# Optimization experiments

Measured on AMD Instinct MI355X. Metric: run time of the kernel, lower is better.

The kernel has to match this reference:

```python
import jax, jax.numpy as jnp
import numpy as np

GRID_H = 64
GRID_W = 64


def make_grid(h, w):
    # torch.meshgrid([arange(h), arange(w)], indexing='xy') -> shape (w, h);
    # grid[i, j] = (j + 0.5, i + 0.5). With h == w == 64 this is square.
    gx, gy = jnp.meshgrid(jnp.arange(h, dtype=jnp.float32),
                          jnp.arange(w, dtype=jnp.float32), indexing='xy')
    return jnp.stack([gx, gy], axis=-1) + 0.5  # (w, h, 2)


def setup_inputs() -> dict:
    key = jax.random.key(0)
    k1, k2 = jax.random.split(key)
    x = jax.random.normal(k1, (4, 128, 64, 64), dtype=jnp.float32)
    y = jax.random.normal(k2, (4, 128, 64, 64), dtype=jnp.float32)
    return {"x": x, "y": y}


def reference(x, y):
    b, c, hx, wx = x.shape
    _, _, hy, wy = y.shape
    scale = c ** (-0.5)
    grids = make_grid(GRID_H, GRID_W)[:hy, :wy].reshape(-1, 2)  # (hy*wy, 2)

    x_ = x.reshape(b, c, hx * wx)
    y_ = y.reshape(b, c, hy * wy)
    # (b, q, k) attention over all key pixels
    attn = jax.nn.softmax(jnp.einsum('bcq,bck->bqk', x_, y_) * scale, axis=-1)
    uv = jnp.einsum('bqk,kt->bqt', attn, grids)  # (b, hx*wx, 2)
    uv = uv.reshape(b, hx, wx, 2)
    # normalize to [-1, 1]
    norm = jnp.asarray([wy, hy], dtype=uv.dtype)
    uv = uv / norm * 2.0 - 1.0
    return uv
```

## Files before the change

### kernel.cpp

```cpp
#include <hip/hip_runtime.h>
#include <math.h>

typedef __attribute__((ext_vector_type(8))) _Float16 f16x8;
typedef __attribute__((ext_vector_type(4))) float f32x4;

#define NPIX 4096
#define C_DIM 128
#define SCALE2 0.12752064638518208f

#if __has_builtin(__builtin_amdgcn_exp2f)
#define EXP2(x) __builtin_amdgcn_exp2f(x)
#else
#define EXP2(x) exp2f(x)
#endif

#define WS_NEED ((size_t)4 << 20)

__global__ __launch_bounds__(256) void conv_y(const float* __restrict__ y,
                                              char* __restrict__ ws)
{
    __shared__ float T[32][132];
    const int wg  = blockIdx.x;
    const int xcd = wg & 7;
    const int b   = xcd >> 1;
    const int sl  = ((xcd & 1) << 6) | (wg >> 3);
    const int k0  = sl * 32;
    const int t   = threadIdx.x;

    {
        const int c = t >> 1, half = t & 1;
        const float* srow = y + ((size_t)b * C_DIM + c) * NPIX + k0 + half * 16;
        float4 rv[4];
        #pragma unroll
        for (int u = 0; u < 4; ++u) rv[u] = *(const float4*)(srow + u * 4);
        #pragma unroll
        for (int u = 0; u < 4; ++u) {
            T[half * 16 + u * 4 + 0][c] = rv[u].x;
            T[half * 16 + u * 4 + 1][c] = rv[u].y;
            T[half * 16 + u * 4 + 2][c] = rv[u].z;
            T[half * 16 + u * 4 + 3][c] = rv[u].w;
        }
    }
    __syncthreads();

    char* panel = ws + (size_t)b * (NPIX * 256);
    const int k = t >> 3, g2 = t & 7;
    f16x8 v0, v1;
    #pragma unroll
    for (int m = 0; m < 8; ++m) {
        v0[m] = (_Float16)T[k][g2 * 16 + m];
        v1[m] = (_Float16)T[k][g2 * 16 + 8 + m];
    }
    const int key = k0 + k, s = key & 7;
    char* drow = panel + (size_t)key * 256;
    *(f16x8*)(drow + (((2 * g2)     ^ s) << 4)) = v0;
    *(f16x8*)(drow + (((2 * g2 + 1) ^ s) << 4)) = v1;
}

__global__ __launch_bounds__(512) void uv_main(const char* __restrict__ ws,
                                               const float* __restrict__ x,
                                               float* __restrict__ out)
{
    __shared__ __align__(16) char Ys[3][32768];

    const int t = threadIdx.x, w = t >> 6, l = t & 63;
    const int n16 = l & 15, quad = l >> 4;
    const int wg  = blockIdx.x;
    const int xcd = wg & 7;
    const int b   = xcd >> 1;
    const int qt  = ((xcd & 1) << 5) | (wg >> 3);
    const int q0  = qt * 64;

    f16x8 bx[4][4];
    {
        const float* xq = x + (size_t)b * C_DIM * NPIX + q0 + n16;
        #pragma unroll
        for (int cc = 0; cc < 4; ++cc)
            #pragma unroll
            for (int qg = 0; qg < 4; ++qg) {
                f16x8 hh;
                #pragma unroll
                for (int j = 0; j < 8; ++j)
                    hh[j] = (_Float16)(xq[(size_t)(cc * 32 + quad * 8 + j) * NPIX + qg * 16] * SCALE2);
                bx[cc][qg] = hh;
            }
    }

    const char* panel = ws + (size_t)b * (NPIX * 256);

    const int arow = w * 16 + n16;
    int aoff[4];
    #pragma unroll
    for (int cc = 0; cc < 4; ++cc)
        aoff[cc] = arow * 256 + (((cc * 4 + quad) ^ (n16 & 7)) << 4);

    int soff[4];
    #pragma unroll
    for (int i = 0; i < 4; ++i) soff[i] = (w * 16 + i * 4) * 256 + l * 16;

    #pragma unroll
    for (int pb = 0; pb < 2; ++pb) {
        const char* gt = panel + (size_t)pb * 32768;
        #pragma unroll
        for (int i = 0; i < 4; ++i)
            __builtin_amdgcn_global_load_lds(
                (const __attribute__((address_space(1))) void*)(gt + soff[i]),
                (__attribute__((address_space(3))) void*)(&Ys[pb][soff[i]]), 16, 0, 0);
    }

    float gxv[4];
    #pragma unroll
    for (int r = 0; r < 4; ++r) gxv[r] = (float)((w & 3) * 16 + quad * 4 + r) + 0.5f;
    const float gyw = (float)(w >> 2) + 0.5f;
    float den[4] = {0.f, 0.f, 0.f, 0.f}, nu[4] = {0.f, 0.f, 0.f, 0.f}, nv[4] = {0.f, 0.f, 0.f, 0.f};

    int bufc = 0;
    for (int kt = 0; kt < 32; ++kt) {
        char* cur = Ys[bufc];

        if (kt < 30) {
            int bufn = bufc + 2; if (bufn >= 3) bufn -= 3;
            const char* gt = panel + (size_t)(kt + 2) * 32768;
            char* nb = Ys[bufn];
            #pragma unroll
            for (int i = 0; i < 4; ++i)
                __builtin_amdgcn_global_load_lds(
                    (const __attribute__((address_space(1))) void*)(gt + soff[i]),
                    (__attribute__((address_space(3))) void*)(&nb[soff[i]]), 16, 0, 0);
            __builtin_amdgcn_s_waitcnt(0x0F78);
        } else {
            __builtin_amdgcn_s_waitcnt(0x0F70);
        }

        f32x4 acc[4];
        #pragma unroll
        for (int qg = 0; qg < 4; ++qg) acc[qg] = (f32x4){0.f, 0.f, 0.f, 0.f};

        #pragma unroll
        for (int cc = 0; cc < 4; ++cc) {
            const f16x8 A = *(const f16x8*)(cur + aoff[cc]);
            #pragma unroll
            for (int qg = 0; qg < 4; ++qg)
                acc[qg] = __builtin_amdgcn_mfma_f32_16x16x32_f16(A, bx[cc][qg], acc[qg], 0, 0, 0);
        }

        const float gy = 2.0f * (float)kt + gyw;
        #pragma unroll
        for (int qg = 0; qg < 4; ++qg) {
            float ps = 0.f, pc = 0.f;
            #pragma unroll
            for (int r = 0; r < 4; ++r) {
                const float p = EXP2(acc[qg][r]);
                ps += p;
                pc += p * gxv[r];
            }
            den[qg] += ps;
            nu[qg]  += pc;
            nv[qg]  += gy * ps;
        }
        ++bufc; if (bufc >= 3) bufc -= 3;
    }

    #pragma unroll
    for (int qg = 0; qg < 4; ++qg) {
        #pragma unroll
        for (int mk = 16; mk <= 32; mk <<= 1) {
            den[qg] += __shfl_xor(den[qg], mk);
            nu[qg]  += __shfl_xor(nu[qg],  mk);
            nv[qg]  += __shfl_xor(nv[qg],  mk);
        }
    }
    __syncthreads();
    float* red = (float*)&Ys[0][0];
    if (quad == 0) {
        #pragma unroll
        for (int qg = 0; qg < 4; ++qg) {
            const int base = (w * 64 + qg * 16 + n16) * 3;
            red[base + 0] = den[qg];
            red[base + 1] = nu[qg];
            red[base + 2] = nv[qg];
        }
    }
    __syncthreads();
    if (t < 64) {
        float d = 0.f, u = 0.f, v = 0.f;
        #pragma unroll
        for (int ww = 0; ww < 8; ++ww) {
            d += red[(ww * 64 + t) * 3 + 0];
            u += red[(ww * 64 + t) * 3 + 1];
            v += red[(ww * 64 + t) * 3 + 2];
        }
        const float inv = 1.0f / d;
        *(float2*)(out + ((size_t)b * NPIX + q0 + t) * 2) =
            make_float2(u * inv * 0.03125f - 1.0f, v * inv * 0.03125f - 1.0f);
    }
}

__global__ __launch_bounds__(256, 2) void uv_attn_kernel(
    const float* __restrict__ x, const float* __restrict__ y, float* __restrict__ out)
{
    __shared__ float Xs[C_DIM][32];
    __shared__ float Ysf[64][128];
    const float SCALE = 0.08838834764831845f;
    const int tid = threadIdx.x;
    const int wgid = blockIdx.x;
    const int xcd = wgid & 7;
    const int b = xcd & 3;
    const int q0 = (((xcd >> 2) << 6) | (wgid >> 3)) * 32;
    const float* xb = x + (size_t)b * C_DIM * NPIX + q0;
    {
        const int cr = tid >> 3;
        const int cc = (tid & 7) << 2;
        #pragma unroll
        for (int i = 0; i < 4; ++i) {
            float4 v = *(const float4*)(xb + (size_t)(cr + (i << 5)) * NPIX + cc);
            v.x *= SCALE; v.y *= SCALE; v.z *= SCALE; v.w *= SCALE;
            *(float4*)(&Xs[cr + (i << 5)][cc]) = v;
        }
    }
    const int rg = tid >> 4;
    const int lane16 = tid & 15;
    const int r0 = rg << 1;
    const int col0 = lane16 << 3;
    float gxv[8];
    #pragma unroll
    for (int j2 = 0; j2 < 8; ++j2) gxv[j2] = (float)((col0 & 63) + j2) + 0.5f;
    const float gyb = (float)(lane16 >> 3) + 0.5f;
    float m_run[2] = {-INFINITY, -INFINITY};
    float den[2] = {0.f, 0.f}, nu[2] = {0.f, 0.f}, nv[2] = {0.f, 0.f};
    const int yr = tid >> 5;
    const int yc = (tid & 31) << 2;
    const float* ybase = y + (size_t)b * C_DIM * NPIX;
    for (int kt = 0; kt < 32; ++kt) {
        float S[2][8];
        #pragma unroll
        for (int r = 0; r < 2; ++r)
            #pragma unroll
            for (int j2 = 0; j2 < 8; ++j2) S[r][j2] = 0.f;
        #pragma unroll
        for (int cb = 0; cb < 2; ++cb) {
            __syncthreads();
            const float* yt = ybase + (size_t)(cb << 6) * NPIX + kt * 128;
            #pragma unroll
            for (int i = 0; i < 8; ++i)
                *(float4*)(&Ysf[yr + (i << 3)][yc]) =
                    *(const float4*)(yt + (size_t)(yr + (i << 3)) * NPIX + yc);
            __syncthreads();
            const int cbase = cb << 6;
            #pragma unroll 16
            for (int c = 0; c < 64; ++c) {
                const float2 xa = *(const float2*)(&Xs[cbase + c][r0]);
                const float4 ya = *(const float4*)(&Ysf[c][col0]);
                const float4 yb4 = *(const float4*)(&Ysf[c][col0 + 4]);
                S[0][0] += xa.x * ya.x;  S[0][1] += xa.x * ya.y;
                S[0][2] += xa.x * ya.z;  S[0][3] += xa.x * ya.w;
                S[0][4] += xa.x * yb4.x; S[0][5] += xa.x * yb4.y;
                S[0][6] += xa.x * yb4.z; S[0][7] += xa.x * yb4.w;
                S[1][0] += xa.y * ya.x;  S[1][1] += xa.y * ya.y;
                S[1][2] += xa.y * ya.z;  S[1][3] += xa.y * ya.w;
                S[1][4] += xa.y * yb4.x; S[1][5] += xa.y * yb4.y;
                S[1][6] += xa.y * yb4.z; S[1][7] += xa.y * yb4.w;
            }
        }
        const float gy = gyb + 2.0f * (float)kt;
        #pragma unroll
        for (int r = 0; r < 2; ++r) {
            float tmax = S[r][0];
            #pragma unroll
            for (int j2 = 1; j2 < 8; ++j2) tmax = fmaxf(tmax, S[r][j2]);
            #pragma unroll
            for (int mk = 8; mk >= 1; mk >>= 1) tmax = fmaxf(tmax, __shfl_xor(tmax, mk, 16));
            const float mnew = fmaxf(m_run[r], tmax);
            const float alpha = __expf(m_run[r] - mnew);
            m_run[r] = mnew;
            float psum = 0.f, pu = 0.f;
            #pragma unroll
            for (int j2 = 0; j2 < 8; ++j2) {
                const float p = __expf(S[r][j2] - mnew);
                psum += p; pu += p * gxv[j2];
            }
            den[r] = den[r] * alpha + psum;
            nu[r] = nu[r] * alpha + pu;
            nv[r] = nv[r] * alpha + gy * psum;
        }
    }
    #pragma unroll
    for (int r = 0; r < 2; ++r)
        #pragma unroll
        for (int mk = 8; mk >= 1; mk >>= 1) {
            den[r] += __shfl_xor(den[r], mk, 16);
            nu[r] += __shfl_xor(nu[r], mk, 16);
            nv[r] += __shfl_xor(nv[r], mk, 16);
        }
    if (lane16 == 0) {
        #pragma unroll
        for (int r = 0; r < 2; ++r) {
            const float inv = 1.0f / den[r];
            const int q = q0 + r0 + r;
            *(float2*)(out + ((size_t)b * NPIX + q) * 2) =
                make_float2(nu[r] * inv * 0.03125f - 1.0f, nv[r] * inv * 0.03125f - 1.0f);
        }
    }
}

extern "C" void kernel_launch(void* const* d_in, const int* in_sizes, int n_in,
                              void* d_out, int out_size, void* d_ws, size_t ws_size,
                              hipStream_t stream) {
    const float* x = (const float*)d_in[0];
    const float* y = (const float*)d_in[1];
    float* out = (float*)d_out;
    if (ws_size >= WS_NEED) {
        hipLaunchKernelGGL(conv_y, dim3(512), dim3(256), 0, stream, y, (char*)d_ws);
        hipLaunchKernelGGL(uv_main, dim3(256), dim3(512), 0, stream,
                           (const char*)d_ws, x, out);
    } else {
        hipLaunchKernelGGL(uv_attn_kernel, dim3(512), dim3(256), 0, stream, x, y, out);
    }
}
```

Baseline: 90.77 us.

## Pre-convert x to fp16 panels and replicate y panels per XCD

After: 97.32 us. 7.2% more time.

```diff
diff --git a/kernel.cpp b/kernel.cpp
--- a/kernel.cpp
+++ b/kernel.cpp
@@ -14,22 +14,30 @@
 #define EXP2(x) exp2f(x)
 #endif
 
-#define WS_NEED ((size_t)4 << 20)
-
-__global__ __launch_bounds__(256) void conv_y(const float* __restrict__ y,
-                                              char* __restrict__ ws)
+#define WS_XP  ((size_t)8 << 20)
+#define WS_NEED ((size_t)12 << 20)
+
+__global__ __launch_bounds__(256) void conv_all(const float* __restrict__ x,
+                                                const float* __restrict__ y,
+                                                char* __restrict__ ws)
 {
     __shared__ float T[32][132];
-    const int wg  = blockIdx.x;
-    const int xcd = wg & 7;
+    const int id  = blockIdx.x;
+    const int isX = (id >= 1024);
+    const int id2 = isX ? (id - 1024) : id;
+    const int xcd = id2 & 7;
     const int b   = xcd >> 1;
-    const int sl  = ((xcd & 1) << 6) | (wg >> 3);
+    const int sl  = isX ? (((xcd & 1) << 6) | (id2 >> 3)) : (id2 >> 3);
     const int k0  = sl * 32;
-    const int t   = threadIdx.x;
+    const float* src = isX ? x : y;
+    char* dst = isX ? (ws + WS_XP + (size_t)b * (1 << 20))
+                    : (ws + (size_t)xcd * (1 << 20));
+    const float sc = isX ? SCALE2 : 1.0f;
+    const int t = threadIdx.x;
 
     {
         const int c = t >> 1, half = t & 1;
-        const float* srow = y + ((size_t)b * C_DIM + c) * NPIX + k0 + half * 16;
+        const float* srow = src + ((size_t)b * C_DIM + c) * NPIX + k0 + half * 16;
         float4 rv[4];
         #pragma unroll
         for (int u = 0; u < 4; ++u) rv[u] = *(const float4*)(srow + u * 4);
@@ -43,22 +51,21 @@
     }
     __syncthreads();
 
-    char* panel = ws + (size_t)b * (NPIX * 256);
     const int k = t >> 3, g2 = t & 7;
     f16x8 v0, v1;
     #pragma unroll
     for (int m = 0; m < 8; ++m) {
-        v0[m] = (_Float16)T[k][g2 * 16 + m];
-        v1[m] = (_Float16)T[k][g2 * 16 + 8 + m];
-    }
-    const int key = k0 + k, s = key & 7;
-    char* drow = panel + (size_t)key * 256;
+        v0[m] = (_Float16)(T[k][g2 * 16 + m] * sc);
+        v1[m] = (_Float16)(T[k][g2 * 16 + 8 + m] * sc);
+    }
+    const int key = k0 + k;
+    const int s = isX ? 0 : (key & 7);
+    char* drow = dst + (size_t)key * 256;
     *(f16x8*)(drow + (((2 * g2)     ^ s) << 4)) = v0;
     *(f16x8*)(drow + (((2 * g2 + 1) ^ s) << 4)) = v1;
 }
 
 __global__ __launch_bounds__(512) void uv_main(const char* __restrict__ ws,
-                                               const float* __restrict__ x,
                                                float* __restrict__ out)
 {
     __shared__ __align__(16) char Ys[3][32768];
@@ -71,22 +78,16 @@
     const int qt  = ((xcd & 1) << 5) | (wg >> 3);
     const int q0  = qt * 64;
 
+    const char* xp = ws + WS_XP + (size_t)b * (1 << 20) + (size_t)q0 * 256;
     f16x8 bx[4][4];
-    {
-        const float* xq = x + (size_t)b * C_DIM * NPIX + q0 + n16;
-        #pragma unroll
-        for (int cc = 0; cc < 4; ++cc)
-            #pragma unroll
-            for (int qg = 0; qg < 4; ++qg) {
-                f16x8 hh;
-                #pragma unroll
-                for (int j = 0; j < 8; ++j)
-                    hh[j] = (_Float16)(xq[(size_t)(cc * 32 + quad * 8 + j) * NPIX + qg * 16] * SCALE2);
-                bx[cc][qg] = hh;
-            }
-    }
-
-    const char* panel = ws + (size_t)b * (NPIX * 256);
+    #pragma unroll
+    for (int cc = 0; cc < 4; ++cc)
+        #pragma unroll
+        for (int qg = 0; qg < 4; ++qg)
+            bx[cc][qg] = *(const f16x8*)(xp + (size_t)(qg * 16 + n16) * 256
+                                            + (cc * 4 + quad) * 16);
+
+    const char* panel = ws + (size_t)xcd * (1 << 20);
 
     const int arow = w * 16 + n16;
     int aoff[4];
@@ -310,9 +311,9 @@
     const float* y = (const float*)d_in[1];
     float* out = (float*)d_out;
     if (ws_size >= WS_NEED) {
-        hipLaunchKernelGGL(conv_y, dim3(512), dim3(256), 0, stream, y, (char*)d_ws);
+        hipLaunchKernelGGL(conv_all, dim3(1536), dim3(256), 0, stream, x, y, (char*)d_ws);
         hipLaunchKernelGGL(uv_main, dim3(256), dim3(512), 0, stream,
-                           (const char*)d_ws, x, out);
+                           (const char*)d_ws, out);
     } else {
         hipLaunchKernelGGL(uv_attn_kernel, dim3(512), dim3(256), 0, stream, x, y, out);
     }
```

## Load key operand directly from global into registers instead of LDS staging

Applied to the files above, without the earlier changes.

Measured after the change: 98.65 us. +8.7%, slower.

```diff
diff --git a/kernel.cpp b/kernel.cpp
--- a/kernel.cpp
+++ b/kernel.cpp
@@ -51,17 +51,16 @@
         v0[m] = (_Float16)T[k][g2 * 16 + m];
         v1[m] = (_Float16)T[k][g2 * 16 + 8 + m];
     }
-    const int key = k0 + k, s = key & 7;
-    char* drow = panel + (size_t)key * 256;
-    *(f16x8*)(drow + (((2 * g2)     ^ s) << 4)) = v0;
-    *(f16x8*)(drow + (((2 * g2 + 1) ^ s) << 4)) = v1;
+    char* drow = panel + (size_t)(k0 + k) * 256;
+    *(f16x8*)(drow + (2 * g2)     * 16) = v0;
+    *(f16x8*)(drow + (2 * g2 + 1) * 16) = v1;
 }
 
 __global__ __launch_bounds__(512) void uv_main(const char* __restrict__ ws,
                                                const float* __restrict__ x,
                                                float* __restrict__ out)
 {
-    __shared__ __align__(16) char Ys[3][32768];
+    __shared__ float red[8 * 64 * 3];
 
     const int t = threadIdx.x, w = t >> 6, l = t & 63;
     const int n16 = l & 15, quad = l >> 4;
@@ -86,27 +85,13 @@
             }
     }
 
-    const char* panel = ws + (size_t)b * (NPIX * 256);
-
-    const int arow = w * 16 + n16;
-    int aoff[4];
+    const char* ap = ws + (size_t)b * (NPIX * 256)
+                   + (size_t)((w * 16 + n16) * 256 + quad * 16);
+
+    f16x8 Ab[2][4];
     #pragma unroll
     for (int cc = 0; cc < 4; ++cc)
-        aoff[cc] = arow * 256 + (((cc * 4 + quad) ^ (n16 & 7)) << 4);
-
-    int soff[4];
-    #pragma unroll
-    for (int i = 0; i < 4; ++i) soff[i] = (w * 16 + i * 4) * 256 + l * 16;
-
-    #pragma unroll
-    for (int pb = 0; pb < 2; ++pb) {
-        const char* gt = panel + (size_t)pb * 32768;
-        #pragma unroll
-        for (int i = 0; i < 4; ++i)
-            __builtin_amdgcn_global_load_lds(
-                (const __attribute__((address_space(1))) void*)(gt + soff[i]),
-                (__attribute__((address_space(3))) void*)(&Ys[pb][soff[i]]), 16, 0, 0);
-    }
+        Ab[0][cc] = *(const f16x8*)(ap + cc * 64);
 
     float gxv[4];
     #pragma unroll
@@ -114,22 +99,15 @@
     const float gyw = (float)(w >> 2) + 0.5f;
     float den[4] = {0.f, 0.f, 0.f, 0.f}, nu[4] = {0.f, 0.f, 0.f, 0.f}, nv[4] = {0.f, 0.f, 0.f, 0.f};
 
-    int bufc = 0;
+    #pragma unroll 2
     for (int kt = 0; kt < 32; ++kt) {
-        char* cur = Ys[bufc];
-
-        if (kt < 30) {
-            int bufn = bufc + 2; if (bufn >= 3) bufn -= 3;
-            const char* gt = panel + (size_t)(kt + 2) * 32768;
-            char* nb = Ys[bufn];
-            #pragma unroll
-            for (int i = 0; i < 4; ++i)
-                __builtin_amdgcn_global_load_lds(
-                    (const __attribute__((address_space(1))) void*)(gt + soff[i]),
-                    (__attribute__((address_space(3))) void*)(&nb[soff[i]]), 16, 0, 0);
-            __builtin_amdgcn_s_waitcnt(0x0F78);
-        } else {
-            __builtin_amdgcn_s_waitcnt(0x0F70);
+        const int cur = kt & 1, nxt = cur ^ 1;
+
+        if (kt < 31) {
+            const char* np = ap + (size_t)(kt + 1) * 32768;
+            #pragma unroll
+            for (int cc = 0; cc < 4; ++cc)
+                Ab[nxt][cc] = *(const f16x8*)(np + cc * 64);
         }
 
         f32x4 acc[4];
@@ -137,12 +115,10 @@
         for (int qg = 0; qg < 4; ++qg) acc[qg] = (f32x4){0.f, 0.f, 0.f, 0.f};
 
         #pragma unroll
-        for (int cc = 0; cc < 4; ++cc) {
-            const f16x8 A = *(const f16x8*)(cur + aoff[cc]);
+        for (int cc = 0; cc < 4; ++cc)
             #pragma unroll
             for (int qg = 0; qg < 4; ++qg)
-                acc[qg] = __builtin_amdgcn_mfma_f32_16x16x32_f16(A, bx[cc][qg], acc[qg], 0, 0, 0);
-        }
+                acc[qg] = __builtin_amdgcn_mfma_f32_16x16x32_f16(Ab[cur][cc], bx[cc][qg], acc[qg], 0, 0, 0);
 
         const float gy = 2.0f * (float)kt + gyw;
         #pragma unroll
@@ -158,7 +134,6 @@
             nu[qg]  += pc;
             nv[qg]  += gy * ps;
         }
-        ++bufc; if (bufc >= 3) bufc -= 3;
     }
 
     #pragma unroll
@@ -170,8 +145,6 @@
             nv[qg]  += __shfl_xor(nv[qg],  mk);
         }
     }
-    __syncthreads();
-    float* red = (float*)&Ys[0][0];
     if (quad == 0) {
         #pragma unroll
         for (int qg = 0; qg < 4; ++qg) {
```

## Split key range across workgroups with 128-query tiles and a merge pass

Applied to the files above, without the earlier changes.

Result: slower. 94.91 us (+4.6%).

```diff
diff --git a/kernel.cpp b/kernel.cpp
--- a/kernel.cpp
+++ b/kernel.cpp
@@ -68,16 +68,17 @@
     const int wg  = blockIdx.x;
     const int xcd = wg & 7;
     const int b   = xcd >> 1;
-    const int qt  = ((xcd & 1) << 5) | (wg >> 3);
-    const int q0  = qt * 64;
-
-    f16x8 bx[4][4];
+    const int ks  = xcd & 1;
+    const int qt  = wg >> 3;
+    const int q0  = qt * 128;
+
+    f16x8 bx[4][8];
     {
         const float* xq = x + (size_t)b * C_DIM * NPIX + q0 + n16;
         #pragma unroll
         for (int cc = 0; cc < 4; ++cc)
             #pragma unroll
-            for (int qg = 0; qg < 4; ++qg) {
+            for (int qg = 0; qg < 8; ++qg) {
                 f16x8 hh;
                 #pragma unroll
                 for (int j = 0; j < 8; ++j)
@@ -86,7 +87,7 @@
             }
     }
 
-    const char* panel = ws + (size_t)b * (NPIX * 256);
+    const char* gsrc = ws + (size_t)b * (NPIX * 256) + (size_t)ks * (2048 * 256);
 
     const int arow = w * 16 + n16;
     int aoff[4];
@@ -100,7 +101,7 @@
 
     #pragma unroll
     for (int pb = 0; pb < 2; ++pb) {
-        const char* gt = panel + (size_t)pb * 32768;
+        const char* gt = gsrc + (size_t)pb * 32768;
         #pragma unroll
         for (int i = 0; i < 4; ++i)
             __builtin_amdgcn_global_load_lds(
@@ -111,16 +112,18 @@
     float gxv[4];
     #pragma unroll
     for (int r = 0; r < 4; ++r) gxv[r] = (float)((w & 3) * 16 + quad * 4 + r) + 0.5f;
-    const float gyw = (float)(w >> 2) + 0.5f;
-    float den[4] = {0.f, 0.f, 0.f, 0.f}, nu[4] = {0.f, 0.f, 0.f, 0.f}, nv[4] = {0.f, 0.f, 0.f, 0.f};
+    const float gyw = (float)(ks * 32 + (w >> 2)) + 0.5f;
+    float den[8], nu[8], nv[8];
+    #pragma unroll
+    for (int i = 0; i < 8; ++i) { den[i] = 0.f; nu[i] = 0.f; nv[i] = 0.f; }
 
     int bufc = 0;
-    for (int kt = 0; kt < 32; ++kt) {
+    for (int kt = 0; kt < 16; ++kt) {
         char* cur = Ys[bufc];
 
-        if (kt < 30) {
+        if (kt < 14) {
             int bufn = bufc + 2; if (bufn >= 3) bufn -= 3;
-            const char* gt = panel + (size_t)(kt + 2) * 32768;
+            const char* gt = gsrc + (size_t)(kt + 2) * 32768;
             char* nb = Ys[bufn];
             #pragma unroll
             for (int i = 0; i < 4; ++i)
@@ -132,37 +135,42 @@
             __builtin_amdgcn_s_waitcnt(0x0F70);
         }
 
-        f32x4 acc[4];
-        #pragma unroll
-        for (int qg = 0; qg < 4; ++qg) acc[qg] = (f32x4){0.f, 0.f, 0.f, 0.f};
-
-        #pragma unroll
-        for (int cc = 0; cc < 4; ++cc) {
-            const f16x8 A = *(const f16x8*)(cur + aoff[cc]);
-            #pragma unroll
-            for (int qg = 0; qg < 4; ++qg)
-                acc[qg] = __builtin_amdgcn_mfma_f32_16x16x32_f16(A, bx[cc][qg], acc[qg], 0, 0, 0);
-        }
+        f16x8 A[4];
+        #pragma unroll
+        for (int cc = 0; cc < 4; ++cc) A[cc] = *(const f16x8*)(cur + aoff[cc]);
 
         const float gy = 2.0f * (float)kt + gyw;
         #pragma unroll
-        for (int qg = 0; qg < 4; ++qg) {
-            float ps = 0.f, pc = 0.f;
-            #pragma unroll
-            for (int r = 0; r < 4; ++r) {
-                const float p = EXP2(acc[qg][r]);
-                ps += p;
-                pc += p * gxv[r];
+        for (int half = 0; half < 2; ++half) {
+            f32x4 acc[4];
+            #pragma unroll
+            for (int q2 = 0; q2 < 4; ++q2) acc[q2] = (f32x4){0.f, 0.f, 0.f, 0.f};
+            #pragma unroll
+            for (int cc = 0; cc < 4; ++cc)
+                #pragma unroll
+                for (int q2 = 0; q2 < 4; ++q2)
+                    acc[q2] = __builtin_amdgcn_mfma_f32_16x16x32_f16(A[cc], bx[cc][half * 4 + q2], acc[q2], 0, 0, 0);
+
+            #pragma unroll
+            for (int q2 = 0; q2 < 4; ++q2) {
+                float ps = 0.f, pc = 0.f;
+                #pragma unroll
+                for (int r = 0; r < 4; ++r) {
+                    const float p = EXP2(acc[q2][r]);
+                    ps += p;
+                    pc += p * gxv[r];
+                }
+                const int qg = half * 4 + q2;
+                den[qg] += ps;
+                nu[qg]  += pc;
+                nv[qg]  += gy * ps;
             }
-            den[qg] += ps;
-            nu[qg]  += pc;
-            nv[qg]  += gy * ps;
         }
         ++bufc; if (bufc >= 3) bufc -= 3;
     }
 
     #pragma unroll
-    for (int qg = 0; qg < 4; ++qg) {
+    for (int qg = 0; qg < 8; ++qg) {
         #pragma unroll
         for (int mk = 16; mk <= 32; mk <<= 1) {
             den[qg] += __shfl_xor(den[qg], mk);
@@ -174,26 +182,40 @@
     float* red = (float*)&Ys[0][0];
     if (quad == 0) {
         #pragma unroll
-        for (int qg = 0; qg < 4; ++qg) {
-            const int base = (w * 64 + qg * 16 + n16) * 3;
+        for (int qg = 0; qg < 8; ++qg) {
+            const int base = (w * 128 + qg * 16 + n16) * 3;
             red[base + 0] = den[qg];
             red[base + 1] = nu[qg];
             red[base + 2] = nv[qg];
         }
     }
     __syncthreads();
-    if (t < 64) {
+    if (t < 128) {
         float d = 0.f, u = 0.f, v = 0.f;
         #pragma unroll
         for (int ww = 0; ww < 8; ++ww) {
-            d += red[(ww * 64 + t) * 3 + 0];
-            u += red[(ww * 64 + t) * 3 + 1];
-            v += red[(ww * 64 + t) * 3 + 2];
-        }
-        const float inv = 1.0f / d;
-        *(float2*)(out + ((size_t)b * NPIX + q0 + t) * 2) =
-            make_float2(u * inv * 0.03125f - 1.0f, v * inv * 0.03125f - 1.0f);
-    }
+            d += red[(ww * 128 + t) * 3 + 0];
+            u += red[(ww * 128 + t) * 3 + 1];
+            v += red[(ww * 128 + t) * 3 + 2];
+        }
+        float* pp = (float*)(ws + (size_t)(NPIX * 256) * 4 - (size_t)(1 << 20))
+                  + ((size_t)((b * 32 + qt) * 128 + t) * 2 + ks) * 3;
+        pp[0] = d; pp[1] = u; pp[2] = v;
+    }
+}
+
+__global__ __launch_bounds__(256) void merge_k(const char* __restrict__ ws,
+                                               float* __restrict__ out)
+{
+    const int id = blockIdx.x * 256 + threadIdx.x;
+    const float* p = (const float*)(ws + (size_t)(NPIX * 256) * 4 - (size_t)(1 << 20))
+                   + (size_t)id * 6;
+    const float d = p[0] + p[3];
+    const float u = p[1] + p[4];
+    const float v = p[2] + p[5];
+    const float inv = 1.0f / d;
+    out[(size_t)id * 2 + 0] = u * inv * 0.03125f - 1.0f;
+    out[(size_t)id * 2 + 1] = v * inv * 0.03125f - 1.0f;
 }
 
 __global__ __launch_bounds__(256, 2) void uv_attn_kernel(
@@ -303,6 +325,9 @@
     }
 }
 
+#undef WS_NEED
+#define WS_NEED ((size_t)5 << 20)
+
 extern "C" void kernel_launch(void* const* d_in, const int* in_sizes, int n_in,
                               void* d_out, int out_size, void* d_ws, size_t ws_size,
                               hipStream_t stream) {
@@ -313,6 +338,8 @@
         hipLaunchKernelGGL(conv_y, dim3(512), dim3(256), 0, stream, y, (char*)d_ws);
         hipLaunchKernelGGL(uv_main, dim3(256), dim3(512), 0, stream,
                            (const char*)d_ws, x, out);
+        hipLaunchKernelGGL(merge_k, dim3(64), dim3(256), 0, stream,
+                           (const char*)d_ws, out);
     } else {
         hipLaunchKernelGGL(uv_attn_kernel, dim3(512), dim3(256), 0, stream, x, y, out);
     }
```
